# Kernel tuning notes

Measured on AMD Instinct MI355X. Metric: run time of the kernel, lower is better.

## Reference

```python
import jax, jax.numpy as jnp
import numpy as np

N, E, C_IN, C_HID, C_OUT = 50000, 800000, 128, 128, 128


def _mlp2(x, w1, b1, w2, b2):
    # build_mlp: 2 layers, no layer norm, plain_last=False -> ReLU after both
    h = jax.nn.relu(x @ w1 + b1)
    return jax.nn.relu(h @ w2 + b2)


def setup_inputs() -> dict:
    key = jax.random.key(0)
    ks = jax.random.split(key, 16)
    s = 0.05
    inp = {
        "x": jax.random.normal(ks[0], (N, C_IN), jnp.float32),
        "pos": jax.random.normal(ks[1], (N, C_IN), jnp.float32),
        "edge_index": jax.random.randint(ks[2], (2, E), 0, N, jnp.int64),
        # lin_in (with bias)
        "W_in": jax.random.normal(ks[3], (C_IN, C_IN), jnp.float32) * s,
        "b_in": jnp.zeros((C_IN,), jnp.float32),
        # PointTransformerConv linear maps (bias=False in PyG)
        "W_lin": jax.random.normal(ks[4], (C_IN, C_OUT), jnp.float32) * s,
        "W_src": jax.random.normal(ks[5], (C_IN, C_OUT), jnp.float32) * s,
        "W_dst": jax.random.normal(ks[6], (C_IN, C_OUT), jnp.float32) * s,
        # pos_nn: in_channels -> hidden -> out_channels
        "pos_w1": jax.random.normal(ks[7], (C_IN, C_HID), jnp.float32) * s,
        "pos_b1": jnp.zeros((C_HID,), jnp.float32),
        "pos_w2": jax.random.normal(ks[8], (C_HID, C_OUT), jnp.float32) * s,
        "pos_b2": jnp.zeros((C_OUT,), jnp.float32),
        # attn_nn: out_channels -> hidden -> out_channels
        "att_w1": jax.random.normal(ks[9], (C_OUT, C_HID), jnp.float32) * s,
        "att_b1": jnp.zeros((C_HID,), jnp.float32),
        "att_w2": jax.random.normal(ks[10], (C_HID, C_OUT), jnp.float32) * s,
        "att_b2": jnp.zeros((C_OUT,), jnp.float32),
        # lin_out (with bias)
        "W_out": jax.random.normal(ks[11], (C_OUT, C_OUT), jnp.float32) * s,
        "b_out": jnp.zeros((C_OUT,), jnp.float32),
    }
    return inp


def reference(x, pos, edge_index, W_in, b_in, W_lin, W_src, W_dst,
              pos_w1, pos_b1, pos_w2, pos_b2,
              att_w1, att_b1, att_w2, att_b2, W_out, b_out):
    n = x.shape[0]
    src, dst = edge_index[0], edge_index[1]  # j -> i

    h = jax.nn.relu(x @ W_in + b_in)                 # [N, C_IN]
    q = h @ W_dst                                    # dest queries
    k = h @ W_src                                    # source keys
    v = h @ W_lin                                    # values

    delta = _mlp2(pos[dst] - pos[src], pos_w1, pos_b1, pos_w2, pos_b2)  # [E, C_OUT]
    alpha = _mlp2(q[dst] - k[src] + delta, att_w1, att_b1, att_w2, att_b2)

    # per-channel segment softmax over destination nodes
    m = jax.ops.segment_max(alpha, dst, num_segments=n)
    m = jnp.where(jnp.isfinite(m), m, 0.0)
    ea = jnp.exp(alpha - m[dst])
    z = jax.ops.segment_sum(ea, dst, num_segments=n)
    attn = ea / (z[dst] + 1e-16)

    msg = attn * (v[src] + delta)                    # [E, C_OUT]
    agg = jax.ops.segment_sum(msg, dst, num_segments=n)

    return jax.nn.relu(agg @ W_out + b_out)
```

## Files before the change

kernel.cpp:

```cpp
#include <hip/hip_runtime.h>
#include <hip/hip_bf16.h>

#define C 128
#define THREADS 256
#define TILE 64
#define EPW 16
#define GTILES 8
#define LDSPAD 8
#define LDSW (C + LDSPAD)

typedef unsigned short ushortT;
typedef __attribute__((ext_vector_type(8))) short short8;
typedef __attribute__((ext_vector_type(8))) ushortT ushort8;
typedef __attribute__((ext_vector_type(4))) float floatx4;
typedef __attribute__((ext_vector_type(4))) unsigned uintx4;

__device__ __forceinline__ unsigned pk2(float a, float b) {
    float2 f; f.x = a; f.y = b;
    union { unsigned u; __hip_bfloat162 h; } cv; cv.h = __float22bfloat162_rn(f);
    return cv.u;
}
__device__ __forceinline__ ushortT f2bf(float x) {
    return (ushortT)(pk2(x, x) & 0xffffu);
}
__device__ __forceinline__ float bf2f(ushortT h) {
    union { unsigned u; float f; } v; v.u = ((unsigned)h) << 16;
    return v.f;
}
__device__ __forceinline__ float2 upk2(unsigned u) {
    union { unsigned u; __hip_bfloat162 h; } cv; cv.u = u;
    return __bfloat1622float2(cv.h);
}
__device__ __forceinline__ void atomic_add_f32(float* p, float v) {
    __hip_atomic_fetch_add(p, v, __ATOMIC_RELAXED, __HIP_MEMORY_SCOPE_AGENT);
}

__device__ __forceinline__ void zero_acc(float acc[8][4]) {
#pragma unroll
    for (int j = 0; j < 8; ++j)
#pragma unroll
        for (int i = 0; i < 4; ++i) acc[j][i] = 0.f;
}

__device__ __forceinline__ void tile_gemm(const float* __restrict__ s_in,
                                          const float* __restrict__ W,
                                          float acc[8][4], int rg, int oc0)
{
#pragma unroll 2
    for (int kc = 0; kc < C; kc += 4) {
        const float4 w0 = *(const float4*)(W + (kc + 0) * C + oc0);
        const float4 w1 = *(const float4*)(W + (kc + 1) * C + oc0);
        const float4 w2 = *(const float4*)(W + (kc + 2) * C + oc0);
        const float4 w3 = *(const float4*)(W + (kc + 3) * C + oc0);
#pragma unroll
        for (int j = 0; j < 8; ++j) {
            const float4 a = *(const float4*)(s_in + (rg * 8 + j) * C + kc);
            acc[j][0] = fmaf(a.w, w3.x, fmaf(a.z, w2.x, fmaf(a.y, w1.x, fmaf(a.x, w0.x, acc[j][0]))));
            acc[j][1] = fmaf(a.w, w3.y, fmaf(a.z, w2.y, fmaf(a.y, w1.y, fmaf(a.x, w0.y, acc[j][1]))));
            acc[j][2] = fmaf(a.w, w3.z, fmaf(a.z, w2.z, fmaf(a.y, w1.z, fmaf(a.x, w0.z, acc[j][2]))));
            acc[j][3] = fmaf(a.w, w3.w, fmaf(a.z, w2.w, fmaf(a.y, w1.w, fmaf(a.x, w0.w, acc[j][3]))));
        }
    }
}

__device__ __forceinline__ void bias_relu(float acc[8][4], const float* __restrict__ b, int oc0) {
    const float4 bv = *(const float4*)(b + oc0);
#pragma unroll
    for (int j = 0; j < 8; ++j) {
        acc[j][0] = fmaxf(acc[j][0] + bv.x, 0.f);
        acc[j][1] = fmaxf(acc[j][1] + bv.y, 0.f);
        acc[j][2] = fmaxf(acc[j][2] + bv.z, 0.f);
        acc[j][3] = fmaxf(acc[j][3] + bv.w, 0.f);
    }
}

__device__ __forceinline__ void wave_gemm(const ushortT (*A)[LDSW],
                                          const ushortT* __restrict__ Bp,
                                          int quad, int m16, int lane,
                                          floatx4 acc[8])
{
#pragma unroll
    for (int nt = 0; nt < 8; ++nt) { acc[nt][0]=0.f; acc[nt][1]=0.f; acc[nt][2]=0.f; acc[nt][3]=0.f; }
#pragma unroll 1
    for (int ks = 0; ks < 4; ++ks) {
        const short8 af = *(const short8*)&A[m16][ks * 32 + quad * 8];
        const ushortT* bpk = Bp + (size_t)ks * 4096 + (size_t)lane * 8;
#pragma unroll
        for (int nt = 0; nt < 8; ++nt) {
            const short8 bf = *(const short8*)(bpk + nt * 512);
            acc[nt] = __builtin_amdgcn_mfma_f32_16x16x32_bf16(af, bf, acc[nt], 0, 0, 0);
        }
    }
}

__device__ __forceinline__ void cstore_relu_r(ushortT (*A)[LDSW], floatx4 acc[8],
                                              const float bias[8], int quad, int m16)
{
#pragma unroll
    for (int nt = 0; nt < 8; ++nt) {
        const float b = bias[nt];
#pragma unroll
        for (int r = 0; r < 4; r += 2) {
            const unsigned p = pk2(fmaxf(acc[nt][r] + b, 0.f), fmaxf(acc[nt][r + 1] + b, 0.f));
            A[quad * 4 + r][nt * 16 + m16]     = (ushortT)(p & 0xffffu);
            A[quad * 4 + r + 1][nt * 16 + m16] = (ushortT)(p >> 16);
        }
    }
}

__device__ __forceinline__ ushortT pack_one(const float* __restrict__ W, int u) {
    const int j = u & 7, lane = (u >> 3) & 63, f = u >> 9;
    const int nt = f & 7, ks = f >> 3;
    const int n = nt * 16 + (lane & 15);
    const int k = ks * 32 + (lane >> 4) * 8 + j;
    return f2bf(W[k * C + n]);
}

extern "C" __global__ void __launch_bounds__(256)
prep1(const float* __restrict__ pw1, const float* __restrict__ pw2,
      const float* __restrict__ aw1, const float* __restrict__ aw2,
      const float* __restrict__ Wd,  const float* __restrict__ Wsrc,
      const float* __restrict__ Wl,  const float* __restrict__ Win,
      const float* __restrict__ pos, ushortT* __restrict__ pos_bf,
      const int* __restrict__ ei, int* __restrict__ deg,
      ushortT* __restrict__ Bpack, ushortT* __restrict__ Bpack2, int N, int E)
{
    const int nb_cvt = (N * 32 + 255) / 256;
    const int b = blockIdx.x, tid = threadIdx.x;
    if (b < 256) {
        const int t = b * 256 + tid;
        const int s = t >> 14;
        const float* W = (s == 0) ? pw1 : (s == 1) ? pw2 : (s == 2) ? aw1 : aw2;
        Bpack[t] = pack_one(W, t & 16383);
    } else if (b < 512) {
        const int t = (b - 256) * 256 + tid;
        const int s = t >> 14;
        const float* W = (s == 0) ? Wd : (s == 1) ? Wsrc : (s == 2) ? Wl : Win;
        Bpack2[t] = pack_one(W, t & 16383);
    } else if (b < 512 + nb_cvt) {
        const int i = (b - 512) * 256 + tid;
        if (i < N * 32) {
            const float4 v = ((const float4*)pos)[i];
            uint2 o; o.x = pk2(v.x, v.y); o.y = pk2(v.z, v.w);
            ((uint2*)pos_bf)[i] = o;
        }
    } else {
        const int e = (b - 512 - nb_cvt) * 256 + tid;
        if (e < E) atomicAdd(&deg[ei[E + e]], 1);
    }
}

extern "C" __global__ void __launch_bounds__(1024)
k_scan(const int* __restrict__ deg, int* __restrict__ off, int n)
{
    __shared__ int part[1024];
    const int t = threadIdx.x;
    const int chunk = (((n + 1023) / 1024) + 3) & ~3;
    const int lo = t * chunk, hi = min(lo + chunk, n);
    int s = 0;
    for (int i = lo; i < hi; i += 4) {
        const int4 d4 = *(const int4*)(deg + i);
        s += d4.x + d4.y + d4.z + d4.w;
    }
    part[t] = s;
    __syncthreads();
    for (int d = 1; d < 1024; d <<= 1) {
        int v = (t >= d) ? part[t - d] : 0;
        __syncthreads();
        part[t] += v;
        __syncthreads();
    }
    int run = (t == 0) ? 0 : part[t - 1];
    for (int i = lo; i < hi; i += 4) {
        const int4 d4 = *(const int4*)(deg + i);
        int4 o;
        o.x = run;
        o.y = o.x + d4.x;
        o.z = o.y + d4.y;
        o.w = o.z + d4.z;
        *(int4*)(off + i) = o;
        run = o.w + d4.w;
    }
}

extern "C" __global__ void __launch_bounds__(256)
prep2(const float* __restrict__ x, const float* __restrict__ b_in,
      const ushortT* __restrict__ Bp2, const ushortT* __restrict__ Bpk,
      const float* __restrict__ pb1, const ushortT* __restrict__ pos_bf,
      ushortT* __restrict__ q_bf, ushortT* __restrict__ k_bf, ushortT* __restrict__ v_bf,
      ushortT* __restrict__ Pd_arr, ushortT* __restrict__ Ps_arr,
      const int* __restrict__ ei, const int* __restrict__ offp, int* __restrict__ curp,
      int* __restrict__ ss, int* __restrict__ sd, int N, int E, int nb_node)
{
    __shared__ ushortT xs[TILE][LDSW];
    __shared__ ushortT hs[TILE][LDSW];
    const int b = blockIdx.x, tx = threadIdx.x;

    if (b >= nb_node) {
        const int e = (b - nb_node) * 256 + tx;
        if (e < E) {
            const int d = ei[E + e];
            const int p = offp[d] + atomicAdd(&curp[d], 1);
            ss[p] = ei[e];
            sd[p] = d;
        }
        return;
    }

    const int rg = tx >> 5;
    const int oc0 = (tx & 31) << 2;
    const int row0 = b * TILE;

#pragma unroll
    for (int j = 0; j < 8; ++j) {
        const int r = rg * 8 + j, n = row0 + r;
        float4 xv; xv.x = xv.y = xv.z = xv.w = 0.f;
        if (n < N) xv = *(const float4*)(x + (size_t)n * C + oc0);
        *(unsigned*)&xs[r][oc0]     = pk2(xv.x, xv.y);
        *(unsigned*)&xs[r][oc0 + 2] = pk2(xv.z, xv.w);
    }

    const int wv = tx >> 6, lane = tx & 63;
    const int quad = lane >> 4, m16 = lane & 15;
    const int row = lane >> 2, li = lane & 3;

    float binv[8];
#pragma unroll
    for (int nt = 0; nt < 8; ++nt) binv[nt] = b_in[nt * 16 + m16];

    const ushortT (*Ax)[LDSW] = (const ushortT (*)[LDSW])&xs[wv * 16];
    ushortT (*Ah)[LDSW] = (ushortT (*)[LDSW])&hs[wv * 16];

    floatx4 macc[8];
    wave_gemm(Ax, Bp2 + (size_t)3 * 16384, quad, m16, lane, macc);
    cstore_relu_r(Ah, macc, binv, quad, m16);

    __syncthreads();

    ushortT (*OS)[LDSW] = (ushortT (*)[LDSW])&xs[wv * 16];
    ushortT* outs[3];
    outs[0] = q_bf; outs[1] = k_bf; outs[2] = v_bf;

    const int nrow = row0 + wv * 16 + row;

#pragma unroll 1
    for (int m = 0; m < 3; ++m) {
        wave_gemm((const ushortT (*)[LDSW])Ah, Bp2 + (size_t)m * 16384, quad, m16, lane, macc);
#pragma unroll
        for (int nt = 0; nt < 8; ++nt) {
#pragma unroll
            for (int r = 0; r < 4; r += 2) {
                const unsigned p = pk2(macc[nt][r], macc[nt][r + 1]);
                OS[quad * 4 + r][nt * 16 + m16]     = (ushortT)(p & 0xffffu);
                OS[quad * 4 + r + 1][nt * 16 + m16] = (ushortT)(p >> 16);
            }
        }
        if (nrow < N) {
#pragma unroll
            for (int i = 0; i < 4; ++i) {
                const ushort8 v8 = *(const ushort8*)&OS[row][i * 32 + li * 8];
                *(ushort8*)(outs[m] + (size_t)nrow * C + i * 32 + li * 8) = v8;
            }
        }
    }

    __syncthreads();
    {
        const ushortT* srcp = pos_bf + (size_t)min(nrow, N - 1) * C;
#pragma unroll
        for (int i = 0; i < 4; ++i) {
            const ushort8 v8 = *(const ushort8*)(srcp + i * 32 + li * 8);
            *(ushort8*)&hs[wv * 16 + row][i * 32 + li * 8] = v8;
        }
    }
    __syncthreads();
    wave_gemm((const ushortT (*)[LDSW])Ah, Bpk , quad, m16, lane, macc);

    float b1v[8];
#pragma unroll
    for (int nt = 0; nt < 8; ++nt) b1v[nt] = pb1[nt * 16 + m16];

#pragma unroll
    for (int nt = 0; nt < 8; ++nt) {
#pragma unroll
        for (int r = 0; r < 4; r += 2) {
            const unsigned p = pk2(macc[nt][r] + b1v[nt], macc[nt][r + 1] + b1v[nt]);
            OS[quad * 4 + r][nt * 16 + m16]     = (ushortT)(p & 0xffffu);
            OS[quad * 4 + r + 1][nt * 16 + m16] = (ushortT)(p >> 16);
        }
    }
    if (nrow < N) {
#pragma unroll
        for (int i = 0; i < 4; ++i) {
            const ushort8 v8 = *(const ushort8*)&OS[row][i * 32 + li * 8];
            *(ushort8*)(Pd_arr + (size_t)nrow * C + i * 32 + li * 8) = v8;
        }
    }
    __syncthreads();
#pragma unroll
    for (int nt = 0; nt < 8; ++nt) {
#pragma unroll
        for (int r = 0; r < 4; r += 2) {
            const unsigned p = pk2(macc[nt][r], macc[nt][r + 1]);
            OS[quad * 4 + r][nt * 16 + m16]     = (ushortT)(p & 0xffffu);
            OS[quad * 4 + r + 1][nt * 16 + m16] = (ushortT)(p >> 16);
        }
    }
    if (nrow < N) {
#pragma unroll
        for (int i = 0; i < 4; ++i) {
            const ushort8 v8 = *(const ushort8*)&OS[row][i * 32 + li * 8];
            *(ushort8*)(Ps_arr + (size_t)nrow * C + i * 32 + li * 8) = v8;
        }
    }
}

__device__ __forceinline__ void gather4(const ushortT* __restrict__ base, int node, int li,
                                        ushort8 dst[4])
{
    const ushort8* p = (const ushort8*)(base + (size_t)node * C) + li;
    dst[0] = p[0]; dst[1] = p[4]; dst[2] = p[8]; dst[3] = p[12];
}

extern "C" __global__ void __launch_bounds__(THREADS)
edge_mfma(const ushortT* __restrict__ Pd_arr, const ushortT* __restrict__ Ps_arr,
          const int* __restrict__ ss, const int* __restrict__ sd,
          const ushortT* __restrict__ q_bf, const ushortT* __restrict__ k_bf,
          const ushortT* __restrict__ v_bf, const ushortT* __restrict__ Bpack,
          const float* __restrict__ pb2,
          const float* __restrict__ ab1, const float* __restrict__ ab2,
          float* __restrict__ z, float* __restrict__ aggU, int E)
{
    __shared__ ushortT Aslab[4][EPW][LDSW];
    __shared__ ushortT Vslab[4][EPW][LDSW];
    __shared__ int     Dslab[4][EPW];
    const int tid = threadIdx.x;
    const int wv = tid >> 6, lane = tid & 63;
    const int quad = lane >> 4, m16 = lane & 15;
    const int row = lane >> 2, li = lane & 3;
    ushortT (*A)[LDSW] = Aslab[wv];
    ushortT (*V)[LDSW] = Vslab[wv];

    float pb2v[8], ab1v[8], ab2v[8];
#pragma unroll
    for (int nt = 0; nt < 8; ++nt) {
        pb2v[nt] = pb2[nt * 16 + m16];
        ab1v[nt] = ab1[nt * 16 + m16]; ab2v[nt] = ab2[nt * 16 + m16];
    }

    const ushortT* B1 = Bpack + 16384;
    const ushortT* B2 = Bpack + 32768;
    const ushortT* B3 = Bpack + 49152;

    const int wave_base = (blockIdx.x * 4 + wv) * (GTILES * EPW);

    const int c2 = lane * 2;
    int   cur_dst = -1;
    float zs0 = 0.f, zs1 = 0.f, gs0 = 0.f, gs1 = 0.f;

    int es, ed, sdr[4];
    {
        const int eidx = min(wave_base + row, E - 1);
        es = ss[eidx]; ed = sd[eidx];
#pragma unroll
        for (int r = 0; r < 4; ++r)
            sdr[r] = sd[min(wave_base + quad * 4 + r, E - 1)];
    }

#pragma unroll 1
    for (int t = 0; t < GTILES; ++t) {
        const int e_base = wave_base + t * EPW;
        if (m16 == 0) {
#pragma unroll
            for (int r = 0; r < 4; ++r) Dslab[wv][quad * 4 + r] = sdr[r];
        }

        ushort8 Pd[4], Ps[4], Qv[4], Kv[4], Vv[4];
        gather4(Pd_arr, ed, li, Pd); gather4(Ps_arr, es, li, Ps);
        gather4(q_bf,  ed, li, Qv); gather4(k_bf,  es, li, Kv);
        gather4(v_bf,  es, li, Vv);

#pragma unroll
        for (int i = 0; i < 4; ++i) {
            const uintx4 pd = *(const uintx4*)&Pd[i];
            const uintx4 ps = *(const uintx4*)&Ps[i];
            uintx4 o;
#pragma unroll
            for (int w = 0; w < 4; ++w) {
                const float2 a = upk2(pd[w]), b = upk2(ps[w]);
                o[w] = pk2(fmaxf(a.x - b.x, 0.f), fmaxf(a.y - b.y, 0.f));
            }
            *(uintx4*)&A[row][i * 32 + li * 8] = o;
            *(ushort8*)&V[row][i * 32 + li * 8] = Vv[i];
        }

        floatx4 acc[8];

        wave_gemm(A, B1, quad, m16, lane, acc);
        unsigned dlp[8][2];
#pragma unroll
        for (int nt = 0; nt < 8; ++nt) {
            const float b = pb2v[nt];
            const unsigned p0 = pk2(fmaxf(acc[nt][0] + b, 0.f), fmaxf(acc[nt][1] + b, 0.f));
            const unsigned p1 = pk2(fmaxf(acc[nt][2] + b, 0.f), fmaxf(acc[nt][3] + b, 0.f));
            dlp[nt][0] = p0; dlp[nt][1] = p1;
            A[quad * 4 + 0][nt * 16 + m16] = (ushortT)(p0 & 0xffffu);
            A[quad * 4 + 1][nt * 16 + m16] = (ushortT)(p0 >> 16);
            A[quad * 4 + 2][nt * 16 + m16] = (ushortT)(p1 & 0xffffu);
            A[quad * 4 + 3][nt * 16 + m16] = (ushortT)(p1 >> 16);
        }

#pragma unroll
        for (int i = 0; i < 4; ++i) {
            const uintx4 dv = *(const uintx4*)&A[row][i * 32 + li * 8];
            const uintx4 qv = *(const uintx4*)&Qv[i];
            const uintx4 kv = *(const uintx4*)&Kv[i];
            uintx4 o;
#pragma unroll
            for (int w = 0; w < 4; ++w) {
                const float2 qq = upk2(qv[w]), kk = upk2(kv[w]), dd = upk2(dv[w]);
                o[w] = pk2(qq.x - kk.x + dd.x, qq.y - kk.y + dd.y);
            }
            *(uintx4*)&A[row][i * 32 + li * 8] = o;
        }

        int nes = es, ned = ed, nsdr[4];
#pragma unroll
        for (int r = 0; r < 4; ++r) nsdr[r] = sdr[r];
        if (t + 1 < GTILES) {
            const int e2 = e_base + EPW;
            const int ei2 = min(e2 + row, E - 1);
            nes = ss[ei2]; ned = sd[ei2];
#pragma unroll
            for (int r = 0; r < 4; ++r)
                nsdr[r] = sd[min(e2 + quad * 4 + r, E - 1)];
        }

        wave_gemm(A, B2, quad, m16, lane, acc);
        cstore_relu_r(A, acc, ab1v, quad, m16);

        wave_gemm(A, B3, quad, m16, lane, acc);
#pragma unroll
        for (int nt = 0; nt < 8; ++nt) {
            const float b = ab2v[nt];
#pragma unroll
            for (int r = 0; r < 4; ++r)
                acc[nt][r] = __expf(fmaxf(acc[nt][r] + b, 0.f));
        }

        if (e_base + EPW > E) {
#pragma unroll
            for (int r = 0; r < 4; ++r)
                if (e_base + quad * 4 + r >= E) {
#pragma unroll
                    for (int nt = 0; nt < 8; ++nt) acc[nt][r] = 0.f;
                }
        }

#pragma unroll
        for (int nt = 0; nt < 8; ++nt) {
#pragma unroll
            for (int r = 0; r < 4; ++r) {
                const float2 dpair = upk2(dlp[nt][r >> 1]);
                const float dlv = (r & 1) ? dpair.y : dpair.x;
                const int ridx = quad * 4 + r, cidx = nt * 16 + m16;
                const float vv = bf2f(V[ridx][cidx]);
                V[ridx][cidx] = f2bf(vv + dlv);
                A[ridx][cidx] = f2bf(acc[nt][r]);
            }
        }

#pragma unroll 4
        for (int e = 0; e < EPW; ++e) {
            const int d = Dslab[wv][e];
            const float2 ea2 = upk2(*(const unsigned*)&A[e][c2]);
            const float2 vp2 = upk2(*(const unsigned*)&V[e][c2]);
            if (d != cur_dst) {
                if (cur_dst >= 0) {
                    float* zp = z    + (size_t)cur_dst * C + c2;
                    float* gp = aggU + (size_t)cur_dst * C + c2;
                    atomic_add_f32(zp,     zs0);
                    atomic_add_f32(zp + 1, zs1);
                    atomic_add_f32(gp,     gs0);
                    atomic_add_f32(gp + 1, gs1);
                }
                cur_dst = d;
                zs0 = ea2.x;           zs1 = ea2.y;
                gs0 = ea2.x * vp2.x;   gs1 = ea2.y * vp2.y;
            } else {
                zs0 += ea2.x;                   zs1 += ea2.y;
                gs0 = fmaf(ea2.x, vp2.x, gs0);  gs1 = fmaf(ea2.y, vp2.y, gs1);
            }
        }

        es = nes; ed = ned;
#pragma unroll
        for (int r = 0; r < 4; ++r) sdr[r] = nsdr[r];
    }

    if (cur_dst >= 0) {
        float* zp = z    + (size_t)cur_dst * C + c2;
        float* gp = aggU + (size_t)cur_dst * C + c2;
        atomic_add_f32(zp,     zs0);
        atomic_add_f32(zp + 1, zs1);
        atomic_add_f32(gp,     gs0);
        atomic_add_f32(gp + 1, gs1);
    }
}

extern "C" __global__ void __launch_bounds__(THREADS)
out_kernel(const float* __restrict__ aggU, const float* __restrict__ z,
           const float* __restrict__ W_out, const float* __restrict__ b_out,
           float* __restrict__ out, int N)
{
    __shared__ __align__(16) float s_in[TILE * C];
    const int tx = threadIdx.x;
    const int rg = tx >> 5;
    const int oc0 = (tx & 31) << 2;
    const int row0 = blockIdx.x * TILE;

#pragma unroll
    for (int j = 0; j < 8; ++j) {
        const int r = rg * 8 + j, n = row0 + r;
        float4 a; a.x = a.y = a.z = a.w = 0.f;
        if (n < N) {
            const float4 g  = *(const float4*)(aggU + (size_t)n * C + oc0);
            const float4 zz = *(const float4*)(z    + (size_t)n * C + oc0);
            a.x = g.x / (zz.x + 1e-16f);
            a.y = g.y / (zz.y + 1e-16f);
            a.z = g.z / (zz.z + 1e-16f);
            a.w = g.w / (zz.w + 1e-16f);
        }
        *(float4*)(s_in + r * C + oc0) = a;
    }

    float acc[8][4];
    zero_acc(acc);
    tile_gemm(s_in, W_out, acc, rg, oc0);
    bias_relu(acc, b_out, oc0);
#pragma unroll
    for (int j = 0; j < 8; ++j) {
        const int n = row0 + rg * 8 + j;
        if (n < N) { float4 t; t.x=acc[j][0]; t.y=acc[j][1]; t.z=acc[j][2]; t.w=acc[j][3];
                     *(float4*)(out + (size_t)n * C + oc0) = t; }
    }
}

extern "C" void kernel_launch(void* const* d_in, const int* in_sizes, int n_in,
                              void* d_out, int out_size, void* d_ws, size_t ws_size,
                              hipStream_t stream)
{
    const float* x     = (const float*)d_in[0];
    const float* pos   = (const float*)d_in[1];
    const int*   ei    = (const int*)  d_in[2];
    const float* W_in  = (const float*)d_in[3];
    const float* b_in  = (const float*)d_in[4];
    const float* W_lin = (const float*)d_in[5];
    const float* W_src = (const float*)d_in[6];
    const float* W_dst = (const float*)d_in[7];
    const float* pw1   = (const float*)d_in[8];
    const float* pb1   = (const float*)d_in[9];
    const float* pw2   = (const float*)d_in[10];
    const float* pb2   = (const float*)d_in[11];
    const float* aw1   = (const float*)d_in[12];
    const float* ab1   = (const float*)d_in[13];
    const float* aw2   = (const float*)d_in[14];
    const float* ab2   = (const float*)d_in[15];
    const float* W_out = (const float*)d_in[16];
    const float* b_out = (const float*)d_in[17];

    const int N = in_sizes[0] / C;
    const int E = in_sizes[2] / 2;
    const size_t NC = (size_t)N * C;

    float*   z      = (float*)d_ws;
    float*   aggU   = z + NC;
    ushortT* q_bf   = (ushortT*)(aggU + NC);
    ushortT* k_bf   = q_bf + NC;
    ushortT* v_bf   = k_bf + NC;
    ushortT* Pd_arr = v_bf + NC;
    ushortT* Ps_arr = Pd_arr + NC;
    ushortT* pos_bf = Ps_arr + NC;
    ushortT* Bpack  = pos_bf + NC;
    ushortT* Bpack2 = Bpack + 65536;
    int*     deg    = (int*)(Bpack2 + 65536);
    int*     curp   = deg + N;
    int*     offp   = curp + N;
    int*     ss     = offp + N;
    int*     sdst   = ss + E;

    hipMemsetAsync(z, 0, 2 * NC * sizeof(float), stream);
    hipMemsetAsync(deg, 0, 2 * (size_t)N * sizeof(int), stream);

    const int nb_cvt  = (N * 32 + 255) / 256;
    const int nb_hist = (E + 255) / 256;
    prep1<<<512 + nb_cvt + nb_hist, 256, 0, stream>>>(pw1, pw2, aw1, aw2,
                                                      W_dst, W_src, W_lin, W_in,
                                                      pos, pos_bf, ei, deg,
                                                      Bpack, Bpack2, N, E);

    k_scan<<<1, 1024, 0, stream>>>(deg, offp, N);

    const int nb = (N + TILE - 1) / TILE;
    prep2<<<nb + nb_hist, 256, 0, stream>>>(x, b_in, Bpack2, Bpack, pb1, pos_bf,
                                            q_bf, k_bf, v_bf, Pd_arr, Ps_arr,
                                            ei, offp, curp, ss, sdst, N, E, nb);

    const int edges_per_block = 4 * GTILES * EPW;
    const int eb = (E + edges_per_block - 1) / edges_per_block;
    edge_mfma<<<eb, THREADS, 0, stream>>>(Pd_arr, Ps_arr, ss, sdst, q_bf, k_bf, v_bf, Bpack,
                                          pb2, ab1, ab2, z, aggU, E);
    out_kernel<<<nb, THREADS, 0, stream>>>(aggU, z, W_out, b_out, (float*)d_out, N);
}
```

Measured before the change: 621.1 us.

## Use bf16 MFMA for output projection and fold log2e into attention exp

The output kernel's fp32 FMA tile GEMM is replaced with the shared bf16 MFMA wave_gemm path. W_out is pre-packed into a new bf16 buffer inside prep1, and the normalized aggregate is staged in LDS as bf16. Separately, the second attention-MLP weights and bias are pre-scaled by log2(e), so the edge kernel can call the raw hardware v_exp_f32 (exp2) instead of __expf. This cuts ALU work in the output GEMM and the exponentials, at the cost of bf16 rounding in the final projection and a slightly larger workspace.

```diff
diff --git a/kernel.cpp b/kernel.cpp
--- a/kernel.cpp
+++ b/kernel.cpp
@@ -8,6 +8,7 @@
 #define GTILES 8
 #define LDSPAD 8
 #define LDSW (C + LDSPAD)
+#define LOG2E 1.44269504088896340736f
 
 typedef unsigned short ushortT;
 typedef __attribute__((ext_vector_type(8))) short short8;
@@ -31,47 +32,11 @@
     union { unsigned u; __hip_bfloat162 h; } cv; cv.u = u;
     return __bfloat1622float2(cv.h);
 }
+__device__ __forceinline__ float exp2_hw(float x) {
+    float r; asm("v_exp_f32 %0, %1" : "=v"(r) : "v"(x)); return r;
+}
 __device__ __forceinline__ void atomic_add_f32(float* p, float v) {
     __hip_atomic_fetch_add(p, v, __ATOMIC_RELAXED, __HIP_MEMORY_SCOPE_AGENT);
-}
-
-__device__ __forceinline__ void zero_acc(float acc[8][4]) {
-#pragma unroll
-    for (int j = 0; j < 8; ++j)
-#pragma unroll
-        for (int i = 0; i < 4; ++i) acc[j][i] = 0.f;
-}
-
-__device__ __forceinline__ void tile_gemm(const float* __restrict__ s_in,
-                                          const float* __restrict__ W,
-                                          float acc[8][4], int rg, int oc0)
-{
-#pragma unroll 2
-    for (int kc = 0; kc < C; kc += 4) {
-        const float4 w0 = *(const float4*)(W + (kc + 0) * C + oc0);
-        const float4 w1 = *(const float4*)(W + (kc + 1) * C + oc0);
-        const float4 w2 = *(const float4*)(W + (kc + 2) * C + oc0);
-        const float4 w3 = *(const float4*)(W + (kc + 3) * C + oc0);
-#pragma unroll
-        for (int j = 0; j < 8; ++j) {
-            const float4 a = *(const float4*)(s_in + (rg * 8 + j) * C + kc);
-            acc[j][0] = fmaf(a.w, w3.x, fmaf(a.z, w2.x, fmaf(a.y, w1.x, fmaf(a.x, w0.x, acc[j][0]))));
-            acc[j][1] = fmaf(a.w, w3.y, fmaf(a.z, w2.y, fmaf(a.y, w1.y, fmaf(a.x, w0.y, acc[j][1]))));
-            acc[j][2] = fmaf(a.w, w3.z, fmaf(a.z, w2.z, fmaf(a.y, w1.z, fmaf(a.x, w0.z, acc[j][2]))));
-            acc[j][3] = fmaf(a.w, w3.w, fmaf(a.z, w2.w, fmaf(a.y, w1.w, fmaf(a.x, w0.w, acc[j][3]))));
-        }
-    }
-}
-
-__device__ __forceinline__ void bias_relu(float acc[8][4], const float* __restrict__ b, int oc0) {
-    const float4 bv = *(const float4*)(b + oc0);
-#pragma unroll
-    for (int j = 0; j < 8; ++j) {
-        acc[j][0] = fmaxf(acc[j][0] + bv.x, 0.f);
-        acc[j][1] = fmaxf(acc[j][1] + bv.y, 0.f);
-        acc[j][2] = fmaxf(acc[j][2] + bv.z, 0.f);
-        acc[j][3] = fmaxf(acc[j][3] + bv.w, 0.f);
-    }
 }
 
 __device__ __forceinline__ void wave_gemm(const ushortT (*A)[LDSW],
@@ -121,9 +86,11 @@
       const float* __restrict__ aw1, const float* __restrict__ aw2,
       const float* __restrict__ Wd,  const float* __restrict__ Wsrc,
       const float* __restrict__ Wl,  const float* __restrict__ Win,
+      const float* __restrict__ Wout,
       const float* __restrict__ pos, ushortT* __restrict__ pos_bf,
       const int* __restrict__ ei, int* __restrict__ deg,
-      ushortT* __restrict__ Bpack, ushortT* __restrict__ Bpack2, int N, int E)
+      ushortT* __restrict__ Bpack, ushortT* __restrict__ Bpack2,
+      ushortT* __restrict__ BpackO, int N, int E)
 {
     const int nb_cvt = (N * 32 + 255) / 256;
     const int b = blockIdx.x, tid = threadIdx.x;
@@ -131,21 +98,31 @@
         const int t = b * 256 + tid;
         const int s = t >> 14;
         const float* W = (s == 0) ? pw1 : (s == 1) ? pw2 : (s == 2) ? aw1 : aw2;
-        Bpack[t] = pack_one(W, t & 16383);
+        const int u = t & 16383;
+        const int j = u & 7, lane = (u >> 3) & 63, f = u >> 9;
+        const int nt = f & 7, ks = f >> 3;
+        const int n = nt * 16 + (lane & 15);
+        const int k = ks * 32 + (lane >> 4) * 8 + j;
+        float v = W[k * C + n];
+        if (s == 3) v *= LOG2E;
+        Bpack[t] = f2bf(v);
     } else if (b < 512) {
         const int t = (b - 256) * 256 + tid;
         const int s = t >> 14;
         const float* W = (s == 0) ? Wd : (s == 1) ? Wsrc : (s == 2) ? Wl : Win;
         Bpack2[t] = pack_one(W, t & 16383);
-    } else if (b < 512 + nb_cvt) {
-        const int i = (b - 512) * 256 + tid;
+    } else if (b < 576) {
+        const int t = (b - 512) * 256 + tid;
+        BpackO[t] = pack_one(Wout, t);
+    } else if (b < 576 + nb_cvt) {
+        const int i = (b - 576) * 256 + tid;
         if (i < N * 32) {
             const float4 v = ((const float4*)pos)[i];
             uint2 o; o.x = pk2(v.x, v.y); o.y = pk2(v.z, v.w);
             ((uint2*)pos_bf)[i] = o;
         }
     } else {
-        const int e = (b - 512 - nb_cvt) * 256 + tid;
+        const int e = (b - 576 - nb_cvt) * 256 + tid;
         if (e < E) atomicAdd(&deg[ei[E + e]], 1);
     }
 }
@@ -345,7 +322,8 @@
 #pragma unroll
     for (int nt = 0; nt < 8; ++nt) {
         pb2v[nt] = pb2[nt * 16 + m16];
-        ab1v[nt] = ab1[nt * 16 + m16]; ab2v[nt] = ab2[nt * 16 + m16];
+        ab1v[nt] = ab1[nt * 16 + m16];
+        ab2v[nt] = ab2[nt * 16 + m16] * LOG2E;
     }
 
     const ushortT* B1 = Bpack + 16384;
@@ -445,7 +423,7 @@
             const float b = ab2v[nt];
 #pragma unroll
             for (int r = 0; r < 4; ++r)
-                acc[nt][r] = __expf(fmaxf(acc[nt][r] + b, 0.f));
+                acc[nt][r] = exp2_hw(fmaxf(acc[nt][r] + b, 0.f));
         }
 
         if (e_base + EPW > E) {
@@ -510,10 +488,10 @@
 
 extern "C" __global__ void __launch_bounds__(THREADS)
 out_kernel(const float* __restrict__ aggU, const float* __restrict__ z,
-           const float* __restrict__ W_out, const float* __restrict__ b_out,
+           const ushortT* __restrict__ BpO, const float* __restrict__ b_out,
            float* __restrict__ out, int N)
 {
-    __shared__ __align__(16) float s_in[TILE * C];
+    __shared__ ushortT us[TILE][LDSW];
     const int tx = threadIdx.x;
     const int rg = tx >> 5;
     const int oc0 = (tx & 31) << 2;
@@ -531,18 +509,29 @@
             a.z = g.z / (zz.z + 1e-16f);
             a.w = g.w / (zz.w + 1e-16f);
         }
-        *(float4*)(s_in + r * C + oc0) = a;
-    }
-
-    float acc[8][4];
-    zero_acc(acc);
-    tile_gemm(s_in, W_out, acc, rg, oc0);
-    bias_relu(acc, b_out, oc0);
-#pragma unroll
-    for (int j = 0; j < 8; ++j) {
-        const int n = row0 + rg * 8 + j;
-        if (n < N) { float4 t; t.x=acc[j][0]; t.y=acc[j][1]; t.z=acc[j][2]; t.w=acc[j][3];
-                     *(float4*)(out + (size_t)n * C + oc0) = t; }
+        *(unsigned*)&us[r][oc0]     = pk2(a.x, a.y);
+        *(unsigned*)&us[r][oc0 + 2] = pk2(a.z, a.w);
+    }
+
+    const int wv = tx >> 6, lane = tx & 63;
+    const int quad = lane >> 4, m16 = lane & 15;
+
+    floatx4 macc[8];
+    wave_gemm((const ushortT (*)[LDSW])&us[wv * 16], BpO, quad, m16, lane, macc);
+
+    float bo[8];
+#pragma unroll
+    for (int nt = 0; nt < 8; ++nt) bo[nt] = b_out[nt * 16 + m16];
+
+#pragma unroll
+    for (int r = 0; r < 4; ++r) {
+        const int n = row0 + wv * 16 + quad * 4 + r;
+        if (n < N) {
+            float* op = out + (size_t)n * C + m16;
+#pragma unroll
+            for (int nt = 0; nt < 8; ++nt)
+                op[nt * 16] = fmaxf(macc[nt][r] + bo[nt], 0.f);
+        }
     }
 }
 
@@ -583,7 +572,8 @@
     ushortT* pos_bf = Ps_arr + NC;
     ushortT* Bpack  = pos_bf + NC;
     ushortT* Bpack2 = Bpack + 65536;
-    int*     deg    = (int*)(Bpack2 + 65536);
+    ushortT* BpackO = Bpack2 + 65536;
+    int*     deg    = (int*)(BpackO + 16384);
     int*     curp   = deg + N;
     int*     offp   = curp + N;
     int*     ss     = offp + N;
@@ -594,10 +584,10 @@
 
     const int nb_cvt  = (N * 32 + 255) / 256;
     const int nb_hist = (E + 255) / 256;
-    prep1<<<512 + nb_cvt + nb_hist, 256, 0, stream>>>(pw1, pw2, aw1, aw2,
-                                                      W_dst, W_src, W_lin, W_in,
+    prep1<<<576 + nb_cvt + nb_hist, 256, 0, stream>>>(pw1, pw2, aw1, aw2,
+                                                      W_dst, W_src, W_lin, W_in, W_out,
                                                       pos, pos_bf, ei, deg,
-                                                      Bpack, Bpack2, N, E);
+                                                      Bpack, Bpack2, BpackO, N, E);
 
     k_scan<<<1, 1024, 0, stream>>>(deg, offp, N);
 
@@ -610,5 +600,5 @@
     const int eb = (E + edges_per_block - 1) / edges_per_block;
     edge_mfma<<<eb, THREADS, 0, stream>>>(Pd_arr, Ps_arr, ss, sdst, q_bf, k_bf, v_bf, Bpack,
                                           pb2, ab1, ab2, z, aggU, E);
-    out_kernel<<<nb, THREADS, 0, stream>>>(aggU, z, W_out, b_out, (float*)d_out, N);
-}
+    out_kernel<<<nb, THREADS, 0, stream>>>(aggU, z, BpackO, b_out, (float*)d_out, N);
+}
```

Measured after the change: 603.4 us. 1.03x faster.
